# Performance work log

Hardware: AMD Instinct MI355X
Metric: run time of the kernel (lower is better)

The kernel has to match this reference:

```python
import jax, jax.numpy as jnp
import numpy as np
from jax.ops import segment_sum

EPS = 1e-5
N, E = 100000, 1600000
CIN, H, COUT, ED = 32, 64, 16, 16


def _lin(k, fan_in, fan_out):
    return jax.random.normal(k, (fan_in, fan_out), jnp.float32) / np.sqrt(fan_in)


def setup_inputs() -> dict:
    key = jax.random.key(0)
    ks = jax.random.split(key, 24)
    inp = {
        "x": jax.random.normal(ks[0], (N, CIN), jnp.float32),
        "edge_index": jax.random.randint(ks[1], (2, E), 0, N, jnp.int32),
        "edge_attr": jax.random.normal(ks[2], (E, ED), jnp.float32),
    }
    # layer 1 (SAGEConvWithEdgeAttr: in=CIN -> H)
    inp.update(
        l1_Wl=_lin(ks[3], CIN, H), l1_bl=jnp.zeros((H,), jnp.float32),
        l1_Wr=_lin(ks[4], CIN, H),
        l1_We=_lin(ks[5], ED, H), l1_be=jnp.zeros((H,), jnp.float32),
        l1_Wg=_lin(ks[6], 2 * H, H), l1_bg=jnp.zeros((H,), jnp.float32),
        l1_bng=jnp.ones((H,), jnp.float32), l1_bnb=jnp.zeros((H,), jnp.float32),
    )
    # layer 2 (H -> H)
    inp.update(
        l2_Wl=_lin(ks[7], H, H), l2_bl=jnp.zeros((H,), jnp.float32),
        l2_Wr=_lin(ks[8], H, H),
        l2_We=_lin(ks[9], ED, H), l2_be=jnp.zeros((H,), jnp.float32),
        l2_Wg=_lin(ks[10], 2 * H, H), l2_bg=jnp.zeros((H,), jnp.float32),
        l2_bng=jnp.ones((H,), jnp.float32), l2_bnb=jnp.zeros((H,), jnp.float32),
    )
    # GraphNorms (weight=1, bias=0, mean_scale=1 at init; randomize slightly via ones)
    inp.update(
        gn1_g=jnp.ones((H,), jnp.float32), gn1_b=jnp.zeros((H,), jnp.float32), gn1_a=jnp.ones((H,), jnp.float32),
        gn2_g=jnp.ones((H,), jnp.float32), gn2_b=jnp.zeros((H,), jnp.float32), gn2_a=jnp.ones((H,), jnp.float32),
        lin_W=_lin(ks[11], H, COUT), lin_b=jnp.zeros((COUT,), jnp.float32),
    )
    return inp


def _sage_edge_layer(x, row, col, ea, Wl, bl, Wr, We, be, Wg, bg, bng, bnb):
    n = x.shape[0]
    ea_t = ea @ We + be                                        # [E', H]
    deg = segment_sum(jnp.ones_like(col, dtype=x.dtype), col, num_segments=n)
    agg = segment_sum(x[row], col, num_segments=n) / jnp.maximum(deg, 1.0)[:, None]
    out = agg @ Wl + bl + x @ Wr                               # SAGEConv (mean)
    gate = jax.nn.sigmoid(jnp.concatenate([out[col], ea_t], -1) @ Wg + bg)
    out = out + segment_sum(gate * ea_t, col, num_segments=n)  # edge contributions
    mu = out.mean(0)
    var = ((out - mu) ** 2).mean(0)                            # BatchNorm1d (batch stats)
    out = bng * (out - mu) * jax.lax.rsqrt(var + EPS) + bnb
    return jax.nn.relu(2.0 * out)                              # Identity residual + out, relu


def _graph_norm(x, g, b, a):
    mu = x.mean(0)
    xc = x - a * mu
    var = (xc ** 2).mean(0)
    return g * xc * jax.lax.rsqrt(var + EPS) + b


def reference(x, edge_index, edge_attr,
              l1_Wl, l1_bl, l1_Wr, l1_We, l1_be, l1_Wg, l1_bg, l1_bng, l1_bnb,
              l2_Wl, l2_bl, l2_Wr, l2_We, l2_be, l2_Wg, l2_bg, l2_bng, l2_bnb,
              gn1_g, gn1_b, gn1_a, gn2_g, gn2_b, gn2_a, lin_W, lin_b):
    n = x.shape[0]
    loop = jnp.arange(n, dtype=edge_index.dtype)
    row = jnp.concatenate([edge_index[0], loop])               # add_self_loops
    col = jnp.concatenate([edge_index[1], loop])
    ea = jnp.concatenate([edge_attr, jnp.ones((n, edge_attr.shape[1]), edge_attr.dtype)], 0)
    h = _sage_edge_layer(x, row, col, ea, l1_Wl, l1_bl, l1_Wr, l1_We, l1_be, l1_Wg, l1_bg, l1_bng, l1_bnb)
    h = jax.nn.relu(h)
    h = jax.nn.relu(_graph_norm(h, gn1_g, gn1_b, gn1_a))
    h = _sage_edge_layer(h, row, col, ea, l2_Wl, l2_bl, l2_Wr, l2_We, l2_be, l2_Wg, l2_bg, l2_bng, l2_bnb)
    h = jax.nn.relu(h)
    h = jax.nn.relu(_graph_norm(h, gn2_g, gn2_b, gn2_a))
    return h @ lin_W + lin_b
```

## Files before the change

### kernel.cpp

```cpp
#include <hip/hip_runtime.h>
#include <hip/hip_fp16.h>
#include <math.h>
#include <stdint.h>

#define H 64
#define ED 16
#define CO 16
#define WGRID 2048
#define NWAVES (WGRID * 4)
#define CPART 2048
static constexpr float EPSV = 1e-5f;
static constexpr float LOG2E = 1.44269504f;

typedef _Float16 h2v __attribute__((ext_vector_type(2)));
typedef _Float16 f16x8 __attribute__((ext_vector_type(8)));
typedef float f32x4 __attribute__((ext_vector_type(4)));

__device__ __forceinline__ float sigm2(float z) {
    return __builtin_amdgcn_rcpf(1.0f + __builtin_amdgcn_exp2f(-z));
}

__device__ __forceinline__ h2v as_h2(int x) { union { int i; h2v h; } u; u.i = x; return u.h; }

__device__ __forceinline__ f16x8 as_f16x8(int4 v) { union { int4 i; f16x8 h; } u; u.i = v; return u.h; }

__device__ __forceinline__ int pack2(float a, float b) {
    __half2 h = __floats2half2_rn(a, b);
    return *reinterpret_cast<int*>(&h);
}

__global__ void k_prep(const float* __restrict__ We1, const float* __restrict__ be1, const float* __restrict__ Wg1,
                       const float* __restrict__ We2, const float* __restrict__ be2, const float* __restrict__ Wg2,
                       float* __restrict__ ws) {
    int j = threadIdx.x;
    for (int l = 0; l < 2; ++l) {
        const float* We = l ? We2 : We1;
        const float* be = l ? be2 : be1;
        const float* Wg = l ? Wg2 : Wg1;
        int* wth = (int*)(ws + (l ? 1024 : 0));
        int* wgh = (int*)(ws + (l ? 1536 : 512));
        float* ets = ws + 2048 + l * 192;
        float* vs  = ws + 2112 + l * 192;
        float* dv  = ws + 2176 + l * 192;
        float wt[ED], wg[ED];
        float et = be[j];
        for (int k = 0; k < ED; ++k) { wt[k] = We[k * H + j]; et += wt[k]; }
        ets[j] = et;
        float d = 0.f;
        for (int m = 0; m < H; ++m) d += be[m] * Wg[(H + m) * H + j];
        float vsum = d;
        for (int k = 0; k < ED; ++k) {
            float acc = 0.f;
            for (int m = 0; m < H; ++m) acc += We[k * H + m] * Wg[(H + m) * H + j];
            wg[k] = acc;
            vsum += acc;
        }
        dv[j] = d * LOG2E;
        vs[j] = vsum * LOG2E;
        for (int q = 0; q < 8; ++q) {
            wth[j * 8 + q] = pack2(wt[2 * q], wt[2 * q + 1]);
            wgh[j * 8 + q] = pack2(wg[2 * q] * LOG2E, wg[2 * q + 1] * LOG2E);
        }
    }
    for (int s = 0; s < 8; ++s) ws[2432 + s * 64 + j] = 0.f;
}

__global__ void k_xh(const float* __restrict__ x, __half* __restrict__ xh, int total4) {
    int i = blockIdx.x * blockDim.x + threadIdx.x;
    if (i >= total4) return;
    float4 v = *reinterpret_cast<const float4*>(x + (size_t)i * 4);
    __half2 h0 = __floats2half2_rn(v.x, v.y), h1 = __floats2half2_rn(v.z, v.w);
    uint2 o;
    o.x = *reinterpret_cast<unsigned*>(&h0);
    o.y = *reinterpret_cast<unsigned*>(&h1);
    *reinterpret_cast<uint2*>(xh + (size_t)i * 4) = o;
}

__global__ void k_eah(const float* __restrict__ ea, int4* __restrict__ eah, int E) {
    int e = blockIdx.x * blockDim.x + threadIdx.x;
    if (e >= E) return;
    const float4* src = reinterpret_cast<const float4*>(ea + (size_t)e * ED);
    float4 v0 = src[0], v1 = src[1], v2 = src[2], v3 = src[3];
    int hh[8];
    hh[0] = pack2(v0.x, v0.y); hh[1] = pack2(v0.z, v0.w);
    hh[2] = pack2(v1.x, v1.y); hh[3] = pack2(v1.z, v1.w);
    hh[4] = pack2(v2.x, v2.y); hh[5] = pack2(v2.z, v2.w);
    hh[6] = pack2(v3.x, v3.y); hh[7] = pack2(v3.z, v3.w);
    const int4* o = reinterpret_cast<const int4*>(hh);
    eah[(size_t)e * 2 + 0] = o[0];
    eah[(size_t)e * 2 + 1] = o[1];
}

__global__ void k_count(const int* __restrict__ cols, int* __restrict__ cnt, int E) {
    int e = blockIdx.x * blockDim.x + threadIdx.x;
    if (e < E) atomicAdd(&cnt[cols[e]], 1);
}

__global__ __launch_bounds__(1024) void k_scan1(const int* __restrict__ cnt, int* __restrict__ bs, int N) {
    __shared__ int ls[1024];
    int t = threadIdx.x;
    int i = blockIdx.x * 1024 + t;
    ls[t] = (i < N) ? cnt[i] : 0;
    __syncthreads();
    for (int off = 512; off > 0; off >>= 1) {
        if (t < off) ls[t] += ls[t + off];
        __syncthreads();
    }
    if (t == 0) bs[blockIdx.x] = ls[0];
}

__global__ __launch_bounds__(1024) void k_scan2(int* __restrict__ bs, int SB) {
    __shared__ int ls[1024];
    int t = threadIdx.x;
    int v = (t < SB) ? bs[t] : 0;
    ls[t] = v;
    __syncthreads();
    for (int off = 1; off < 1024; off <<= 1) {
        int x = (t >= off) ? ls[t - off] : 0;
        __syncthreads();
        ls[t] += x;
        __syncthreads();
    }
    if (t < SB) bs[t] = ls[t] - v;
}

__global__ __launch_bounds__(1024) void k_scan3(const int* __restrict__ cnt, const int* __restrict__ bs,
                                                int* __restrict__ rowptr, int N, int E) {
    __shared__ int ls[1024];
    int t = threadIdx.x;
    int i = blockIdx.x * 1024 + t;
    int v = (i < N) ? cnt[i] : 0;
    ls[t] = v;
    __syncthreads();
    for (int off = 1; off < 1024; off <<= 1) {
        int x = (t >= off) ? ls[t - off] : 0;
        __syncthreads();
        ls[t] += x;
        __syncthreads();
    }
    if (i < N) rowptr[i] = bs[blockIdx.x] + ls[t] - v;
    if (i == 0) rowptr[N] = E;
}

__global__ void k_ranges(const int* __restrict__ rowptr, int* __restrict__ ranges, int N, int E, int nw) {
    int w = blockIdx.x * blockDim.x + threadIdx.x;
    if (w > nw) return;
    if (w == nw) { ranges[nw] = N; return; }
    int t0 = (int)((long)E * w / nw);
    int lo = 0, hi = N;
    while (lo < hi) { int mid = (lo + hi) >> 1; if (rowptr[mid] < t0) lo = mid + 1; else hi = mid; }
    ranges[w] = lo;
}

__global__ __launch_bounds__(256) void k_part(const int* __restrict__ rows, const int* __restrict__ cols,
                                              int2* __restrict__ tmp, int* __restrict__ offtab,
                                              int E, int NB, int SH) {
    __shared__ int hist[1025];
    __shared__ int pscan[256];
    __shared__ int2 stage[CPART];
    int tid = threadIdx.x;
    int base = blockIdx.x * CPART;
    int cnt = min(CPART, E - base);
    for (int i = tid; i <= NB; i += 256) hist[i] = 0;
    __syncthreads();
    int myc[8], myr[8];
#pragma unroll
    for (int q = 0; q < 8; ++q) {
        int li = q * 256 + tid;
        if (li < cnt) {
            int e = base + li;
            myc[q] = cols[e];
            myr[q] = rows[e];
            atomicAdd(&hist[myc[q] >> SH], 1);
        } else myc[q] = -1;
    }
    __syncthreads();
    int h[4], s = 0;
    int b0 = tid * 4;
#pragma unroll
    for (int k = 0; k < 4; ++k) { h[k] = (b0 + k < NB) ? hist[b0 + k] : 0; s += h[k]; }
    pscan[tid] = s;
    __syncthreads();
    for (int off = 1; off < 256; off <<= 1) {
        int v = (tid >= off) ? pscan[tid - off] : 0;
        __syncthreads();
        pscan[tid] += v;
        __syncthreads();
    }
    int excl = pscan[tid] - s;
    __syncthreads();
    int run = excl;
#pragma unroll
    for (int k = 0; k < 4; ++k) {
        if (b0 + k < NB) hist[b0 + k] = run;
        run += h[k];
    }
    __syncthreads();
    int* ot = offtab + (size_t)blockIdx.x * (NB + 1);
    for (int i = tid; i < NB; i += 256) ot[i] = hist[i];
    if (tid == 0) ot[NB] = cnt;
    __syncthreads();
    int mask = (1 << SH) - 1;
#pragma unroll
    for (int q = 0; q < 8; ++q) {
        if (myc[q] >= 0) {
            int b = myc[q] >> SH;
            int p = atomicAdd(&hist[b], 1);
            int e = base + q * 256 + tid;
            stage[p] = make_int2(myr[q], (e << SH) | (myc[q] & mask));
        }
    }
    __syncthreads();
    int2* dst = tmp + base;
    for (int i = tid; i < cnt; i += 256) dst[i] = stage[i];
}

__global__ __launch_bounds__(256) void k_build(const int* __restrict__ rowptr, const int2* __restrict__ tmp,
                                               const int* __restrict__ offtab, const int4* __restrict__ eah,
                                               int* __restrict__ erow, __half* __restrict__ eap,
                                               int N, int NB, int SH, int PB) {
    __shared__ int lcur[1024];
    int tid = threadIdx.x;
    int b = blockIdx.x;
    int NPB = 1 << SH;
    int nodelo = b << SH;
    for (int j = tid; j < NPB; j += 256) {
        int n = nodelo + j;
        lcur[j] = (n < N) ? rowptr[n] : 0;
    }
    __syncthreads();
    int mask = NPB - 1;
    for (int i = tid; i < PB; i += 256) {
        const int* ot = offtab + (size_t)i * (NB + 1);
        int j0 = ot[b], j1 = ot[b + 1];
        for (int j = j0; j < j1; ++j) {
            int2 v = tmp[(size_t)i * CPART + j];
            int e = (int)(((unsigned)v.y) >> SH);
            int cl = v.y & mask;
            int p = atomicAdd(&lcur[cl], 1);
            erow[p] = v.x;
            int4 a0 = eah[(size_t)e * 2 + 0];
            int4 a1 = eah[(size_t)e * 2 + 1];
            int4* d = reinterpret_cast<int4*>(eap + (size_t)p * ED);
            d[0] = a0; d[1] = a1;
        }
    }
}

template <int CIN, bool GN>
__global__ __launch_bounds__(256) void k_gather(const __half* __restrict__ x, const int* __restrict__ rowptr,
                         const int* __restrict__ ranges,
                         const int* __restrict__ erow, float* __restrict__ agg,
                         const float* __restrict__ s1, const float* __restrict__ s2,
                         const float* __restrict__ gng, const float* __restrict__ gnb,
                         const float* __restrict__ gna, float Ninv, int N) {
    int lane = threadIdx.x & 63;
    int w = (blockIdx.x * blockDim.x + threadIdx.x) >> 6;
    float A = 1.f, B = 0.f;
    if (GN) {
        float mu = s1[lane] * Ninv, m2 = s2[lane] * Ninv, a = gna[lane];
        float var = m2 - 2.f * a * mu * mu + a * a * mu * mu;
        A = gng[lane] * rsqrtf(var + EPSV);
        B = gnb[lane] - A * a * mu;
    }
    int n0 = ranges[w], n1 = ranges[w + 1];
    for (int n = n0; n < n1; ++n) {
        int s = rowptr[n], te = rowptr[n + 1];
        if (CIN == 64) {
            float raw = __half2float(x[(size_t)n * 64 + lane]);
            float acc = GN ? fmaxf(fmaf(A, raw, B), 0.f) : raw;
            int i = s;
            for (; i + 7 < te; i += 8) {
                int r0 = erow[i],     r1 = erow[i + 1], r2 = erow[i + 2], r3 = erow[i + 3];
                int r4 = erow[i + 4], r5 = erow[i + 5], r6 = erow[i + 6], r7 = erow[i + 7];
                float x0 = __half2float(x[(size_t)r0 * 64 + lane]);
                float x1 = __half2float(x[(size_t)r1 * 64 + lane]);
                float x2 = __half2float(x[(size_t)r2 * 64 + lane]);
                float x3 = __half2float(x[(size_t)r3 * 64 + lane]);
                float x4 = __half2float(x[(size_t)r4 * 64 + lane]);
                float x5 = __half2float(x[(size_t)r5 * 64 + lane]);
                float x6 = __half2float(x[(size_t)r6 * 64 + lane]);
                float x7 = __half2float(x[(size_t)r7 * 64 + lane]);
                if (GN) {
                    x0 = fmaxf(fmaf(A, x0, B), 0.f); x1 = fmaxf(fmaf(A, x1, B), 0.f);
                    x2 = fmaxf(fmaf(A, x2, B), 0.f); x3 = fmaxf(fmaf(A, x3, B), 0.f);
                    x4 = fmaxf(fmaf(A, x4, B), 0.f); x5 = fmaxf(fmaf(A, x5, B), 0.f);
                    x6 = fmaxf(fmaf(A, x6, B), 0.f); x7 = fmaxf(fmaf(A, x7, B), 0.f);
                }
                acc += ((x0 + x1) + (x2 + x3)) + ((x4 + x5) + (x6 + x7));
            }
            for (; i < te; ++i) {
                float xv = __half2float(x[(size_t)erow[i] * 64 + lane]);
                if (GN) xv = fmaxf(fmaf(A, xv, B), 0.f);
                acc += xv;
            }
            agg[(size_t)n * H + lane] = acc;
        } else {
            int c = lane & 31, half = lane >> 5;
            float acc = half ? 0.f : __half2float(x[(size_t)n * 32 + c]);
            int i = s + half;
            for (; i + 6 < te; i += 8) {
                int r0 = erow[i], r1 = erow[i + 2], r2 = erow[i + 4], r3 = erow[i + 6];
                float x0 = __half2float(x[(size_t)r0 * 32 + c]);
                float x1 = __half2float(x[(size_t)r1 * 32 + c]);
                float x2 = __half2float(x[(size_t)r2 * 32 + c]);
                float x3 = __half2float(x[(size_t)r3 * 32 + c]);
                acc += (x0 + x1) + (x2 + x3);
            }
            for (; i < te; i += 2) acc += __half2float(x[(size_t)erow[i] * 32 + c]);
            acc += __shfl_xor(acc, 32);
            if (half == 0) agg[(size_t)n * H + c] = acc;
        }
    }
}

#define MT4A(mq, aval) \
    acc[mq][0] = fmaf(aval, w1.x, acc[mq][0]); acc[mq][1] = fmaf(aval, w1.y, acc[mq][1]); \
    acc[mq][2] = fmaf(aval, w1.z, acc[mq][2]); acc[mq][3] = fmaf(aval, w1.w, acc[mq][3]);
#define MT4X(mq, aval) \
    acc[mq][0] = fmaf(aval, w2.x, acc[mq][0]); acc[mq][1] = fmaf(aval, w2.y, acc[mq][1]); \
    acc[mq][2] = fmaf(aval, w2.z, acc[mq][2]); acc[mq][3] = fmaf(aval, w2.w, acc[mq][3]);

template <int K, bool GN>
__global__ __launch_bounds__(256) void k_gemmfu(
        const float* __restrict__ A,
        const __half* __restrict__ A2, int lda2,
        const float* __restrict__ W1, const float* __restrict__ W2,
        const float* __restrict__ bias,
        const float* __restrict__ Wg, const float* __restrict__ bg,
        const float* __restrict__ s1, const float* __restrict__ s2,
        const float* __restrict__ gng, const float* __restrict__ gnb,
        const float* __restrict__ gna, float Ninv,
        const int* __restrict__ rowptr,
        __half* __restrict__ pre, __half* __restrict__ uout, int N) {
    __shared__ float WA[64 * 64];
    __shared__ float WB[K * 64];
    __shared__ float big[64][68];
    __shared__ float As[64], Bs[64], invd[64];
    int tid = threadIdx.x;
    for (int idx = tid; idx < K * 64; idx += 256) { WA[idx] = W1[idx]; WB[idx] = W2[idx]; }
    int nb = blockIdx.x * 64;
    if (tid < 64) {
        if (GN) {
            float mu = s1[tid] * Ninv, m2 = s2[tid] * Ninv, a = gna[tid];
            float var = m2 - 2.f * a * mu * mu + a * a * mu * mu;
            float Av = gng[tid] * rsqrtf(var + EPSV);
            As[tid] = Av; Bs[tid] = gnb[tid] - Av * a * mu;
        }
        int n = nb + tid;
        invd[tid] = (n < N) ? 1.f / (float)(rowptr[n + 1] - rowptr[n] + 1) : 0.f;
    }
    __syncthreads();
    int tm = tid >> 4, tn = tid & 15;
    int m0 = tm * 4, j0 = tn * 4;
    float acc[4][4];
#pragma unroll
    for (int jq = 0; jq < 4; ++jq) {
        float b = bias[j0 + jq];
#pragma unroll
        for (int mq = 0; mq < 4; ++mq) acc[mq][jq] = b;
    }
    int sn = tid >> 2, kq4 = (tid & 3) * 4;
    int sg = nb + sn;
    for (int k0 = 0; k0 < K; k0 += 16) {
        if (k0) __syncthreads();
        if (sg < N) {
            float4 av = *reinterpret_cast<const float4*>(A + (size_t)sg * 64 + k0 + kq4);
            float sc = invd[sn];
            av.x *= sc; av.y *= sc; av.z *= sc; av.w *= sc;
            big[kq4 + 0][sn] = av.x; big[kq4 + 1][sn] = av.y;
            big[kq4 + 2][sn] = av.z; big[kq4 + 3][sn] = av.w;
            uint2 hv = *reinterpret_cast<const uint2*>(A2 + (size_t)sg * lda2 + k0 + kq4);
            __half2 h01 = *reinterpret_cast<__half2*>(&hv.x);
            __half2 h23 = *reinterpret_cast<__half2*>(&hv.y);
            float2 f01 = __half22float2(h01), f23 = __half22float2(h23);
            float xv0 = f01.x, xv1 = f01.y, xv2 = f23.x, xv3 = f23.y;
            if (GN) {
                xv0 = fmaxf(fmaf(As[k0 + kq4 + 0], xv0, Bs[k0 + kq4 + 0]), 0.f);
                xv1 = fmaxf(fmaf(As[k0 + kq4 + 1], xv1, Bs[k0 + kq4 + 1]), 0.f);
                xv2 = fmaxf(fmaf(As[k0 + kq4 + 2], xv2, Bs[k0 + kq4 + 2]), 0.f);
                xv3 = fmaxf(fmaf(As[k0 + kq4 + 3], xv3, Bs[k0 + kq4 + 3]), 0.f);
            }
            big[16 + kq4 + 0][sn] = xv0; big[16 + kq4 + 1][sn] = xv1;
            big[16 + kq4 + 2][sn] = xv2; big[16 + kq4 + 3][sn] = xv3;
        } else {
#pragma unroll
            for (int q = 0; q < 4; ++q) { big[kq4 + q][sn] = 0.f; big[16 + kq4 + q][sn] = 0.f; }
        }
        __syncthreads();
#pragma unroll
        for (int k = 0; k < 16; ++k) {
            float4 am = *reinterpret_cast<const float4*>(&big[k][m0]);
            float4 w1 = *reinterpret_cast<const float4*>(&WA[(k0 + k) * 64 + j0]);
            MT4A(0, am.x) MT4A(1, am.y) MT4A(2, am.z) MT4A(3, am.w)
            float4 xm = *reinterpret_cast<const float4*>(&big[16 + k][m0]);
            float4 w2 = *reinterpret_cast<const float4*>(&WB[(k0 + k) * 64 + j0]);
            MT4X(0, xm.x) MT4X(1, xm.y) MT4X(2, xm.z) MT4X(3, xm.w)
        }
    }
    __syncthreads();
#pragma unroll
    for (int mq = 0; mq < 4; ++mq) {
        int n = nb + m0 + mq;
        if (n < N) {
            uint2 o;
            o.x = pack2(acc[mq][0], acc[mq][1]);
            o.y = pack2(acc[mq][2], acc[mq][3]);
            *reinterpret_cast<uint2*>(pre + (size_t)n * 64 + j0) = o;
        }
#pragma unroll
        for (int jq = 0; jq < 4; ++jq) big[j0 + jq][m0 + mq] = acc[mq][jq];
    }
    for (int idx = tid; idx < 4096; idx += 256) WA[idx] = Wg[idx] * LOG2E;
    __syncthreads();
    float acc2[4][4];
#pragma unroll
    for (int jq = 0; jq < 4; ++jq) {
        float b = bg[j0 + jq] * LOG2E;
#pragma unroll
        for (int mq = 0; mq < 4; ++mq) acc2[mq][jq] = b;
    }
#pragma unroll 8
    for (int k = 0; k < 64; ++k) {
        float4 pm = *reinterpret_cast<const float4*>(&big[k][m0]);
        float4 w1 = *reinterpret_cast<const float4*>(&WA[k * 64 + j0]);
        acc2[0][0] = fmaf(pm.x, w1.x, acc2[0][0]); acc2[0][1] = fmaf(pm.x, w1.y, acc2[0][1]);
        acc2[0][2] = fmaf(pm.x, w1.z, acc2[0][2]); acc2[0][3] = fmaf(pm.x, w1.w, acc2[0][3]);
        acc2[1][0] = fmaf(pm.y, w1.x, acc2[1][0]); acc2[1][1] = fmaf(pm.y, w1.y, acc2[1][1]);
        acc2[1][2] = fmaf(pm.y, w1.z, acc2[1][2]); acc2[1][3] = fmaf(pm.y, w1.w, acc2[1][3]);
        acc2[2][0] = fmaf(pm.z, w1.x, acc2[2][0]); acc2[2][1] = fmaf(pm.z, w1.y, acc2[2][1]);
        acc2[2][2] = fmaf(pm.z, w1.z, acc2[2][2]); acc2[2][3] = fmaf(pm.z, w1.w, acc2[2][3]);
        acc2[3][0] = fmaf(pm.w, w1.x, acc2[3][0]); acc2[3][1] = fmaf(pm.w, w1.y, acc2[3][1]);
        acc2[3][2] = fmaf(pm.w, w1.z, acc2[3][2]); acc2[3][3] = fmaf(pm.w, w1.w, acc2[3][3]);
    }
#pragma unroll
    for (int mq = 0; mq < 4; ++mq) {
        int n = nb + m0 + mq;
        if (n < N) {
            uint2 o;
            o.x = pack2(acc2[mq][0], acc2[mq][1]);
            o.y = pack2(acc2[mq][2], acc2[mq][3]);
            *reinterpret_cast<uint2*>(uout + (size_t)n * 64 + j0) = o;
        }
    }
}

__global__ __launch_bounds__(256) void k_gate(
        const int* __restrict__ rowptr, const int* __restrict__ ranges,
        const __half* __restrict__ eap,
        const int* __restrict__ wth, const int* __restrict__ wgh,
        const float* __restrict__ be, const float* __restrict__ dv,
        const float* __restrict__ ets, const float* __restrict__ vs,
        const __half* __restrict__ u, __half* __restrict__ pre,
        float* __restrict__ s1, float* __restrict__ s2, int N) {
    __shared__ __align__(16) int4 estage[4][128];
    __shared__ float vbuf[4][16][68];
    __shared__ float ebuf[4][16][68];
    __shared__ float ls[2][4][H];
    int lane = threadIdx.x & 63;
    int wv = threadIdx.x >> 6;
    int w = (blockIdx.x << 2) | wv;
    int g = lane >> 4, li = lane & 15;
    f16x8 Bet[4], Bv[4];
#pragma unroll
    for (int c = 0; c < 4; ++c) {
        int j = c * 16 + li;
        int4 bt = make_int4(0, 0, 0, 0), bv = make_int4(0, 0, 0, 0);
        if (g < 2) {
            bt = *reinterpret_cast<const int4*>(&wth[j * 8 + g * 4]);
            bv = *reinterpret_cast<const int4*>(&wgh[j * 8 + g * 4]);
        }
        Bet[c] = as_f16x8(bt);
        Bv[c] = as_f16x8(bv);
    }
    float be_l = be[lane], dv_l = dv[lane], ets_l = ets[lane], vs_l = vs[lane];
    int n0 = ranges[w], n1 = ranges[w + 1];
    float s = 0.f, ss = 0.f;
    if (n0 < n1) {
        int4* dst = &estage[wv][0];
        const int4* gsrc = reinterpret_cast<const int4*>(eap);
        int e0 = rowptr[n0], e1 = rowptr[n1];
        int n = n0;
        int nend = rowptr[n0 + 1];
        size_t idx = (size_t)n * H + lane;
        float u_l = __half2float(u[idx]);
        float pv = __half2float(pre[idx]);
        int np = min(n + 1, n1 - 1);
        size_t idxn = (size_t)np * H + lane;
        float u_n = __half2float(u[idxn]);
        float pv_n = __half2float(pre[idxn]);
        float acc = sigm2(u_l + vs_l) * ets_l;
        float u2 = u_l + dv_l;
        {
            int bytes = min(64, e1 - e0) * 32;
            int4 p0, p1;
            if (lane * 16 < bytes) p0 = gsrc[(size_t)e0 * 2 + lane];
            if (1024 + lane * 16 < bytes) p1 = gsrc[(size_t)e0 * 2 + 64 + lane];
            if (lane * 16 < bytes) dst[lane] = p0;
            if (1024 + lane * 16 < bytes) dst[64 + lane] = p1;
        }
        for (int c = e0; c < e1; c += 64) {
            int cnt = min(64, e1 - c);
            int nbytes = (c + 64 < e1) ? min(64, e1 - c - 64) * 32 : 0;
            int4 p0, p1;
            if (lane * 16 < nbytes) p0 = gsrc[(size_t)(c + 64) * 2 + lane];
            if (1024 + lane * 16 < nbytes) p1 = gsrc[(size_t)(c + 64) * 2 + 64 + lane];
            for (int tb = 0; tb < cnt; tb += 16) {
                int4 af = make_int4(0, 0, 0, 0);
                if (g < 2) af = dst[(tb + li) * 2 + g];
                f16x8 Af = as_f16x8(af);
                f32x4 z = {0.f, 0.f, 0.f, 0.f};
                f32x4 et0 = __builtin_amdgcn_mfma_f32_16x16x32_f16(Af, Bet[0], z, 0, 0, 0);
                f32x4 et1 = __builtin_amdgcn_mfma_f32_16x16x32_f16(Af, Bet[1], z, 0, 0, 0);
                f32x4 et2 = __builtin_amdgcn_mfma_f32_16x16x32_f16(Af, Bet[2], z, 0, 0, 0);
                f32x4 et3 = __builtin_amdgcn_mfma_f32_16x16x32_f16(Af, Bet[3], z, 0, 0, 0);
                f32x4 vv0 = __builtin_amdgcn_mfma_f32_16x16x32_f16(Af, Bv[0], z, 0, 0, 0);
                f32x4 vv1 = __builtin_amdgcn_mfma_f32_16x16x32_f16(Af, Bv[1], z, 0, 0, 0);
                f32x4 vv2 = __builtin_amdgcn_mfma_f32_16x16x32_f16(Af, Bv[2], z, 0, 0, 0);
                f32x4 vv3 = __builtin_amdgcn_mfma_f32_16x16x32_f16(Af, Bv[3], z, 0, 0, 0);
                int r0 = g * 4;
#pragma unroll
                for (int r = 0; r < 4; ++r) {
                    ebuf[wv][r0 + r][li]      = et0[r];
                    ebuf[wv][r0 + r][16 + li] = et1[r];
                    ebuf[wv][r0 + r][32 + li] = et2[r];
                    ebuf[wv][r0 + r][48 + li] = et3[r];
                    vbuf[wv][r0 + r][li]      = vv0[r];
                    vbuf[wv][r0 + r][16 + li] = vv1[r];
                    vbuf[wv][r0 + r][32 + li] = vv2[r];
                    vbuf[wv][r0 + r][48 + li] = vv3[r];
                }
                int p = tb, pend = min(cnt, tb + 16);
                while (p < pend) {
                    while (c + p == nend) {
                        float tval = pv + acc;
                        pre[idx] = __float2half(tval);
                        s += tval; ss += tval * tval;
                        ++n;
                        idx = idxn; u_l = u_n; pv = pv_n;
                        np = min(n + 1, n1 - 1);
                        idxn = (size_t)np * H + lane;
                        u_n = __half2float(u[idxn]);
                        pv_n = __half2float(pre[idxn]);
                        acc = sigm2(u_l + vs_l) * ets_l;
                        u2 = u_l + dv_l;
                        nend = rowptr[n + 1];
                    }
                    int lim = min(pend, nend - c);
                    for (; p + 1 < lim; p += 2) {
                        float V0 = vbuf[wv][p - tb][lane];
                        float E0 = ebuf[wv][p - tb][lane];
                        float V1 = vbuf[wv][p + 1 - tb][lane];
                        float E1 = ebuf[wv][p + 1 - tb][lane];
                        acc += sigm2(u2 + V0) * (be_l + E0) + sigm2(u2 + V1) * (be_l + E1);
                    }
                    if (p < lim) {
                        float V0 = vbuf[wv][p - tb][lane];
                        float E0 = ebuf[wv][p - tb][lane];
                        acc += sigm2(u2 + V0) * (be_l + E0);
                        ++p;
                    }
                }
            }
            if (lane * 16 < nbytes) dst[lane] = p0;
            if (1024 + lane * 16 < nbytes) dst[64 + lane] = p1;
        }
        for (;;) {
            float tval = pv + acc;
            pre[idx] = __float2half(tval);
            s += tval; ss += tval * tval;
            ++n;
            if (n >= n1) break;
            idx = idxn; u_l = u_n; pv = pv_n;
            np = min(n + 1, n1 - 1);
            idxn = (size_t)np * H + lane;
            u_n = __half2float(u[idxn]);
            pv_n = __half2float(pre[idxn]);
            acc = sigm2(u_l + vs_l) * ets_l;
            u2 = u_l + dv_l;
        }
    }
    ls[0][wv][lane] = s; ls[1][wv][lane] = ss;
    __syncthreads();
    if (threadIdx.x < H) {
        float a = ls[0][0][lane] + ls[0][1][lane] + ls[0][2][lane] + ls[0][3][lane];
        float b = ls[1][0][lane] + ls[1][1][lane] + ls[1][2][lane] + ls[1][3][lane];
        atomicAdd(&s1[lane], a);
        atomicAdd(&s2[lane], b);
    }
}

__global__ void k_apply(const __half* __restrict__ in, __half* __restrict__ outb,
                        const float* __restrict__ bng, const float* __restrict__ bnb,
                        const float* __restrict__ s1b, const float* __restrict__ s2b,
                        float* __restrict__ s1g, float* __restrict__ s2g, float Ninv, int N) {
    int j = threadIdx.x, ty = threadIdx.y;
    __shared__ float As[H], Bs[H];
    if (ty == 0) {
        float mu = s1b[j] * Ninv, var = s2b[j] * Ninv - mu * mu;
        float r = rsqrtf(var + EPSV);
        float A = 2.f * bng[j] * r;
        As[j] = A; Bs[j] = 2.f * (bnb[j] - bng[j] * r * mu);
    }
    __syncthreads();
    float A = As[j], B = Bs[j];
    float s = 0.f, ss = 0.f;
    for (int n = blockIdx.x * 4 + ty; n < N; n += gridDim.x * 4) {
        size_t idx = (size_t)n * H + j;
        float v = fmaxf(fmaf(A, __half2float(in[idx]), B), 0.f);
        outb[idx] = __float2half(v);
        s += v; ss += v * v;
    }
    __shared__ float ls[2][4][H];
    ls[0][ty][j] = s; ls[1][ty][j] = ss;
    __syncthreads();
    if (ty == 0) {
        float a = ls[0][0][j] + ls[0][1][j] + ls[0][2][j] + ls[0][3][j];
        float b = ls[1][0][j] + ls[1][1][j] + ls[1][2][j] + ls[1][3][j];
        atomicAdd(&s1g[j], a);
        atomicAdd(&s2g[j], b);
    }
}

__global__ __launch_bounds__(256) void k_final(const __half* __restrict__ hraw, const float* __restrict__ W,
                        const float* __restrict__ bias,
                        const float* __restrict__ s1, const float* __restrict__ s2,
                        const float* __restrict__ gng, const float* __restrict__ gnb,
                        const float* __restrict__ gna, float Ninv,
                        float* __restrict__ outp, int N) {
    __shared__ float As[H], Bs[H];
    if (threadIdx.x < H) {
        int j = threadIdx.x;
        float mu = s1[j] * Ninv, m2 = s2[j] * Ninv, a = gna[j];
        float var = m2 - 2.f * a * mu * mu + a * a * mu * mu;
        float A = gng[j] * rsqrtf(var + EPSV);
        As[j] = A; Bs[j] = gnb[j] - A * a * mu;
    }
    __syncthreads();
    int n = blockIdx.x * blockDim.x + threadIdx.x;
    if (n >= N) return;
    float o[CO];
#pragma unroll
    for (int t = 0; t < CO; ++t) o[t] = bias[t];
    const __half* hr = hraw + (size_t)n * H;
    for (int m4 = 0; m4 < H / 4; ++m4) {
        uint2 hv = *reinterpret_cast<const uint2*>(hr + m4 * 4);
        __half2 h01 = *reinterpret_cast<__half2*>(&hv.x);
        __half2 h23 = *reinterpret_cast<__half2*>(&hv.y);
        float2 f01 = __half22float2(h01), f23 = __half22float2(h23);
        float hx = fmaxf(fmaf(As[m4*4+0], f01.x, Bs[m4*4+0]), 0.f);
        float hy = fmaxf(fmaf(As[m4*4+1], f01.y, Bs[m4*4+1]), 0.f);
        float hz = fmaxf(fmaf(As[m4*4+2], f23.x, Bs[m4*4+2]), 0.f);
        float hw = fmaxf(fmaf(As[m4*4+3], f23.y, Bs[m4*4+3]), 0.f);
#pragma unroll
        for (int t = 0; t < CO; ++t) {
            o[t] += hx * W[(m4*4+0) * CO + t];
            o[t] += hy * W[(m4*4+1) * CO + t];
            o[t] += hz * W[(m4*4+2) * CO + t];
            o[t] += hw * W[(m4*4+3) * CO + t];
        }
    }
    float* orow = outp + (size_t)n * CO;
#pragma unroll
    for (int t4 = 0; t4 < CO / 4; ++t4)
        reinterpret_cast<float4*>(orow)[t4] = make_float4(o[t4*4+0], o[t4*4+1], o[t4*4+2], o[t4*4+3]);
}

extern "C" void kernel_launch(void* const* d_in, const int* in_sizes, int n_in,
                              void* d_out, int out_size, void* d_ws, size_t ws_size,
                              hipStream_t stream) {
    const float* x     = (const float*)d_in[0];
    const int*   ei    = (const int*)d_in[1];
    const float* ea    = (const float*)d_in[2];
    const float* l1_Wl = (const float*)d_in[3];  const float* l1_bl = (const float*)d_in[4];
    const float* l1_Wr = (const float*)d_in[5];  const float* l1_We = (const float*)d_in[6];
    const float* l1_be = (const float*)d_in[7];  const float* l1_Wg = (const float*)d_in[8];
    const float* l1_bg = (const float*)d_in[9];  const float* l1_bng= (const float*)d_in[10];
    const float* l1_bnb= (const float*)d_in[11];
    const float* l2_Wl = (const float*)d_in[12]; const float* l2_bl = (const float*)d_in[13];
    const float* l2_Wr = (const float*)d_in[14]; const float* l2_We = (const float*)d_in[15];
    const float* l2_be = (const float*)d_in[16]; const float* l2_Wg = (const float*)d_in[17];
    const float* l2_bg = (const float*)d_in[18]; const float* l2_bng= (const float*)d_in[19];
    const float* l2_bnb= (const float*)d_in[20];
    const float* gn1_g = (const float*)d_in[21]; const float* gn1_b = (const float*)d_in[22];
    const float* gn1_a = (const float*)d_in[23];
    const float* gn2_g = (const float*)d_in[24]; const float* gn2_b = (const float*)d_in[25];
    const float* gn2_a = (const float*)d_in[26];
    const float* lin_W = (const float*)d_in[27]; const float* lin_b = (const float*)d_in[28];

    const int N = in_sizes[0] / 32;
    const int E = in_sizes[1] / 2;
    const int* rows = ei;
    const int* cols = ei + E;

    int SH = 7, NPB = 128;
    while (((N + NPB - 1) >> SH) > 1024) { SH++; NPB <<= 1; }
    const int NB = (N + NPB - 1) >> SH;
    const int PB = (E + CPART - 1) / CPART;

    float* w    = (float*)d_ws;
    int* wth1   = (int*)w;
    int* wgh1   = (int*)(w + 512);
    int* wth2   = (int*)(w + 1024);
    int* wgh2   = (int*)(w + 1536);
    float* ets1 = w + 2048; float* vs1 = w + 2112; float* dv1 = w + 2176;
    float* ets2 = w + 2240; float* vs2 = w + 2304; float* dv2 = w + 2368;
    float* stats= w + 2432;

    int* ip     = (int*)(w + 8192);
    int* rowptr = ip;
    int* cnt    = ip + (N + 1);
    int* bs     = cnt + N;
    int* ranges = bs + 1024;
    int* erow   = ranges + (NWAVES + 2);

    uintptr_t pa = (uintptr_t)(erow + E);
    pa = (pa + 255) & ~(uintptr_t)255;
    __half* eap = (__half*)pa;
    uintptr_t px = (uintptr_t)(eap + (size_t)E * ED);
    px = (px + 255) & ~(uintptr_t)255;
    __half* xh = (__half*)px;
    uintptr_t pz = (uintptr_t)(xh + (size_t)N * 32);
    pz = (pz + 255) & ~(uintptr_t)255;

    int2* tmp   = (int2*)pz;
    int* offtab = (int*)(tmp + E);
    uintptr_t pe = (uintptr_t)(offtab + (size_t)PB * (NB + 1));
    pe = (pe + 255) & ~(uintptr_t)255;
    int4* eah = (int4*)pe;

    size_t NB64 = (size_t)N * H;
    float* B0 = (float*)pz;
    __half* Bpre = (__half*)(B0 + NB64);
    __half* Bu   = Bpre + NB64;
    __half* B3h  = Bu + NB64;
    __half* B0h  = (__half*)B0;

    const float Ninv = 1.0f / (float)N;
    dim3 rb(64, 4);
    int egrid = (E + 255) / 256;
    int ngrid = (N + 255) / 256;
    int g64 = (N + 63) / 64;
    const int SB = (N + 1023) >> 10;

    k_prep<<<1, 64, 0, stream>>>(l1_We, l1_be, l1_Wg, l2_We, l2_be, l2_Wg, w);
    k_xh<<<(N * 8 + 255) / 256, 256, 0, stream>>>(x, xh, N * 8);
    k_eah<<<egrid, 256, 0, stream>>>(ea, eah, E);

    hipMemsetAsync(cnt, 0, sizeof(int) * (size_t)N, stream);
    k_count<<<egrid, 256, 0, stream>>>(cols, cnt, E);
    k_scan1<<<SB, 1024, 0, stream>>>(cnt, bs, N);
    k_scan2<<<1, 1024, 0, stream>>>(bs, SB);
    k_scan3<<<SB, 1024, 0, stream>>>(cnt, bs, rowptr, N, E);
    k_ranges<<<(NWAVES + 256) / 256, 256, 0, stream>>>(rowptr, ranges, N, E, NWAVES);
    k_part<<<PB, 256, 0, stream>>>(rows, cols, tmp, offtab, E, NB, SH);
    k_build<<<NB, 256, 0, stream>>>(rowptr, tmp, offtab, eah, erow, eap, N, NB, SH, PB);

    k_gather<32, false><<<WGRID, 256, 0, stream>>>(xh, rowptr, ranges, erow, B0,
                                                   nullptr, nullptr, nullptr, nullptr, nullptr, 0.f, N);
    k_gemmfu<32, false><<<g64, 256, 0, stream>>>(B0, xh, 32, l1_Wl, l1_Wr, l1_bl, l1_Wg, l1_bg,
                                                 nullptr, nullptr, nullptr, nullptr, nullptr, 0.f,
                                                 rowptr, Bpre, Bu, N);
    k_gate<<<WGRID, 256, 0, stream>>>(rowptr, ranges, eap, wth1, wgh1, l1_be, dv1, ets1, vs1,
                                      Bu, Bpre, stats + 0, stats + 64, N);
    k_apply<<<256, rb, 0, stream>>>(Bpre, B3h, l1_bng, l1_bnb, stats + 0, stats + 64,
                                    stats + 128, stats + 192, Ninv, N);

    k_gather<64, true><<<WGRID, 256, 0, stream>>>(B3h, rowptr, ranges, erow, B0,
                                                  stats + 128, stats + 192, gn1_g, gn1_b, gn1_a, Ninv, N);
    k_gemmfu<64, true><<<g64, 256, 0, stream>>>(B0, B3h, 64, l2_Wl, l2_Wr, l2_bl, l2_Wg, l2_bg,
                                                stats + 128, stats + 192, gn1_g, gn1_b, gn1_a, Ninv,
                                                rowptr, Bpre, Bu, N);
    k_gate<<<WGRID, 256, 0, stream>>>(rowptr, ranges, eap, wth2, wgh2, l2_be, dv2, ets2, vs2,
                                      Bu, Bpre, stats + 256, stats + 320, N);
    k_apply<<<256, rb, 0, stream>>>(Bpre, B0h, l2_bng, l2_bnb, stats + 256, stats + 320,
                                    stats + 384, stats + 448, Ninv, N);

    k_final<<<ngrid, 256, 0, stream>>>(B0h, lin_W, lin_b, stats + 384, stats + 448,
                                       gn2_g, gn2_b, gn2_a, Ninv, (float*)d_out, N);
}
```

Baseline: 695.4 us.

## Fold gate biases into MFMA, pack gate operands to fp16 LDS, widen k_build

The edge-attribute bias and the gate's dv offset are folded into the MFMA by putting 1.0 in an unused K slot of the A operand and the biases in the matching B slot. The gate value and edge term are then stored together as one packed half2 in shared memory, which halves LDS footprint and traffic and removes the per-edge bias adds. Separately, k_build now launches 1024-thread blocks instead of 256 so more partitions are scanned in parallel per block. Storing the intermediates in fp16 lowers precision of the gate inputs.

```diff
diff --git a/kernel.cpp b/kernel.cpp
--- a/kernel.cpp
+++ b/kernel.cpp
@@ -215,7 +215,7 @@
     for (int i = tid; i < cnt; i += 256) dst[i] = stage[i];
 }
 
-__global__ __launch_bounds__(256) void k_build(const int* __restrict__ rowptr, const int2* __restrict__ tmp,
+__global__ __launch_bounds__(1024) void k_build(const int* __restrict__ rowptr, const int2* __restrict__ tmp,
                                                const int* __restrict__ offtab, const int4* __restrict__ eah,
                                                int* __restrict__ erow, __half* __restrict__ eap,
                                                int N, int NB, int SH, int PB) {
@@ -224,13 +224,13 @@
     int b = blockIdx.x;
     int NPB = 1 << SH;
     int nodelo = b << SH;
-    for (int j = tid; j < NPB; j += 256) {
+    for (int j = tid; j < NPB; j += 1024) {
         int n = nodelo + j;
         lcur[j] = (n < N) ? rowptr[n] : 0;
     }
     __syncthreads();
     int mask = NPB - 1;
-    for (int i = tid; i < PB; i += 256) {
+    for (int i = tid; i < PB; i += 1024) {
         const int* ot = offtab + (size_t)i * (NB + 1);
         int j0 = ot[b], j1 = ot[b + 1];
         for (int j = j0; j < j1; ++j) {
@@ -454,8 +454,7 @@
         const __half* __restrict__ u, __half* __restrict__ pre,
         float* __restrict__ s1, float* __restrict__ s2, int N) {
     __shared__ __align__(16) int4 estage[4][128];
-    __shared__ float vbuf[4][16][68];
-    __shared__ float ebuf[4][16][68];
+    __shared__ unsigned pvet[4][16][68];
     __shared__ float ls[2][4][H];
     int lane = threadIdx.x & 63;
     int wv = threadIdx.x >> 6;
@@ -472,8 +471,12 @@
         }
         Bet[c] = as_f16x8(bt);
         Bv[c] = as_f16x8(bv);
-    }
-    float be_l = be[lane], dv_l = dv[lane], ets_l = ets[lane], vs_l = vs[lane];
+        if (g == 2) {
+            Bet[c][0] = (_Float16)be[j];
+            Bv[c][0]  = (_Float16)dv[j];
+        }
+    }
+    float ets_l = ets[lane], vs_l = vs[lane];
     int n0 = ranges[w], n1 = ranges[w + 1];
     float s = 0.f, ss = 0.f;
     if (n0 < n1) {
@@ -490,7 +493,6 @@
         float u_n = __half2float(u[idxn]);
         float pv_n = __half2float(pre[idxn]);
         float acc = sigm2(u_l + vs_l) * ets_l;
-        float u2 = u_l + dv_l;
         {
             int bytes = min(64, e1 - e0) * 32;
             int4 p0, p1;
@@ -509,6 +511,7 @@
                 int4 af = make_int4(0, 0, 0, 0);
                 if (g < 2) af = dst[(tb + li) * 2 + g];
                 f16x8 Af = as_f16x8(af);
+                if (g == 2) Af[0] = (_Float16)1.0f;
                 f32x4 z = {0.f, 0.f, 0.f, 0.f};
                 f32x4 et0 = __builtin_amdgcn_mfma_f32_16x16x32_f16(Af, Bet[0], z, 0, 0, 0);
                 f32x4 et1 = __builtin_amdgcn_mfma_f32_16x16x32_f16(Af, Bet[1], z, 0, 0, 0);
@@ -521,14 +524,10 @@
                 int r0 = g * 4;
 #pragma unroll
                 for (int r = 0; r < 4; ++r) {
-                    ebuf[wv][r0 + r][li]      = et0[r];
-                    ebuf[wv][r0 + r][16 + li] = et1[r];
-                    ebuf[wv][r0 + r][32 + li] = et2[r];
-                    ebuf[wv][r0 + r][48 + li] = et3[r];
-                    vbuf[wv][r0 + r][li]      = vv0[r];
-                    vbuf[wv][r0 + r][16 + li] = vv1[r];
-                    vbuf[wv][r0 + r][32 + li] = vv2[r];
-                    vbuf[wv][r0 + r][48 + li] = vv3[r];
+                    pvet[wv][r0 + r][li]      = (unsigned)pack2(vv0[r], et0[r]);
+                    pvet[wv][r0 + r][16 + li] = (unsigned)pack2(vv1[r], et1[r]);
+                    pvet[wv][r0 + r][32 + li] = (unsigned)pack2(vv2[r], et2[r]);
+                    pvet[wv][r0 + r][48 + li] = (unsigned)pack2(vv3[r], et3[r]);
                 }
                 int p = tb, pend = min(cnt, tb + 16);
                 while (p < pend) {
@@ -543,21 +542,20 @@
                         u_n = __half2float(u[idxn]);
                         pv_n = __half2float(pre[idxn]);
                         acc = sigm2(u_l + vs_l) * ets_l;
-                        u2 = u_l + dv_l;
                         nend = rowptr[n + 1];
                     }
                     int lim = min(pend, nend - c);
                     for (; p + 1 < lim; p += 2) {
-                        float V0 = vbuf[wv][p - tb][lane];
-                        float E0 = ebuf[wv][p - tb][lane];
-                        float V1 = vbuf[wv][p + 1 - tb][lane];
-                        float E1 = ebuf[wv][p + 1 - tb][lane];
-                        acc += sigm2(u2 + V0) * (be_l + E0) + sigm2(u2 + V1) * (be_l + E1);
+                        unsigned w0 = pvet[wv][p - tb][lane];
+                        unsigned w1 = pvet[wv][p + 1 - tb][lane];
+                        float2 f0 = __half22float2(*reinterpret_cast<__half2*>(&w0));
+                        float2 f1 = __half22float2(*reinterpret_cast<__half2*>(&w1));
+                        acc += sigm2(u_l + f0.x) * f0.y + sigm2(u_l + f1.x) * f1.y;
                     }
                     if (p < lim) {
-                        float V0 = vbuf[wv][p - tb][lane];
-                        float E0 = ebuf[wv][p - tb][lane];
-                        acc += sigm2(u2 + V0) * (be_l + E0);
+                        unsigned w0 = pvet[wv][p - tb][lane];
+                        float2 f0 = __half22float2(*reinterpret_cast<__half2*>(&w0));
+                        acc += sigm2(u_l + f0.x) * f0.y;
                         ++p;
                     }
                 }
@@ -577,7 +575,6 @@
             u_n = __half2float(u[idxn]);
             pv_n = __half2float(pre[idxn]);
             acc = sigm2(u_l + vs_l) * ets_l;
-            u2 = u_l + dv_l;
         }
     }
     ls[0][wv][lane] = s; ls[1][wv][lane] = ss;
@@ -754,7 +751,7 @@
     k_scan3<<<SB, 1024, 0, stream>>>(cnt, bs, rowptr, N, E);
     k_ranges<<<(NWAVES + 256) / 256, 256, 0, stream>>>(rowptr, ranges, N, E, NWAVES);
     k_part<<<PB, 256, 0, stream>>>(rows, cols, tmp, offtab, E, NB, SH);
-    k_build<<<NB, 256, 0, stream>>>(rowptr, tmp, offtab, eah, erow, eap, N, NB, SH, PB);
+    k_build<<<NB, 1024, 0, stream>>>(rowptr, tmp, offtab, eah, erow, eap, N, NB, SH, PB);
 
     k_gather<32, false><<<WGRID, 256, 0, stream>>>(xh, rowptr, ranges, erow, B0,
                                                    nullptr, nullptr, nullptr, nullptr, nullptr, 0.f, N);
```

Result: faster. 676.5 us (-2.7%).
